# Optimization experiments

Measured on AMD Instinct MI355X. Metric: run time of the kernel, lower is better.

## Reference

```python
import jax, jax.numpy as jnp
import numpy as np

ALPHA = 0.8          # triple vs qualifier mixing weight (StarE/QUAD 'sum' strategy)
NUM_ENT = 200000
NUM_REL = 100        # base relations; with inverses rel table has 2*NUM_REL rows
E_DIR = 500000       # edges per direction; edge_index has 2*E_DIR columns
NQ_DIR = 400000      # qualifier (rel, ent, edge_id) triples per direction
D = 200              # emb_dim == gcn_dim
B = 4096             # batch of statements
QP = 6               # qualifier pairs per statement -> quals_ix is [B, 2*QP]


def setup_inputs() -> dict:
    key = jax.random.key(0)
    ks = jax.random.split(key, 24)
    f = lambda i, shape: jax.random.normal(ks[i], shape, jnp.float32) * 0.05
    inp = {
        "ent_embs": f(0, (NUM_ENT, D)),
        "rel_embs": f(1, (2 * NUM_REL, D)),
    }
    for j, n in enumerate(["w_in1", "w_out1", "w_loop1", "w_rel1", "w_q1",
                           "w_in2", "w_out2", "w_loop2", "w_rel2", "w_q2"]):
        inp[n] = f(2 + j, (D, D))
    inp["loop_rel1"] = f(12, (1, D))
    inp["loop_rel2"] = f(13, (1, D))
    inp["b1"] = jnp.zeros((D,), jnp.float32)
    inp["b2"] = jnp.zeros((D,), jnp.float32)
    src = jax.random.randint(ks[14], (E_DIR,), 0, NUM_ENT)
    dst = jax.random.randint(ks[15], (E_DIR,), 0, NUM_ENT)
    # second half are inverse edges
    inp["edge_index"] = jnp.concatenate([jnp.stack([src, dst]), jnp.stack([dst, src])], axis=1)
    et = jax.random.randint(ks[16], (E_DIR,), 0, NUM_REL)
    inp["edge_type"] = jnp.concatenate([et, et + NUM_REL])
    q_r = jax.random.randint(ks[17], (2 * NQ_DIR,), 0, 2 * NUM_REL)
    q_e = jax.random.randint(ks[18], (2 * NQ_DIR,), 0, NUM_ENT)
    q_eid = jax.random.randint(ks[19], (2 * NQ_DIR,), 0, E_DIR)
    inp["quals"] = jnp.stack([q_r, q_e, q_eid])  # [3, 2*NQ_DIR]
    inp["ent_ix"] = jax.random.randint(ks[20], (B,), 0, NUM_ENT)
    inp["rel_ix"] = jax.random.randint(ks[21], (B,), 0, 2 * NUM_REL)
    qi_r = jax.random.randint(ks[22], (B, QP), 0, 2 * NUM_REL)
    qi_e = jax.random.randint(ks[23], (B, QP), 0, NUM_ENT)
    inp["quals_ix"] = jnp.stack([qi_r, qi_e], axis=-1).reshape(B, 2 * QP)  # alternating rel, ent
    return inp


def _comp(h, r):  # CompGCN 'mult' composition
    return h * r


def _compgcn_conv(x, r, edge_index, edge_type, quals,
                  w_in, w_out, w_loop, w_rel, w_q, loop_rel, bias):
    n_ent = x.shape[0]
    E = edge_index.shape[1] // 2
    NQ = quals.shape[1] // 2
    rel_all = jnp.concatenate([r, loop_rel], axis=0)  # loop relation appended last

    def one_dir(idx, etype, q_r, q_e, q_eid, w):
        src, dst = idx[0], idx[1]
        # qualifier-aware per-edge relation embedding
        q_msg = _comp(x[q_e], rel_all[q_r])                               # [NQ, d]
        q_agg = jax.ops.segment_sum(q_msg, q_eid, num_segments=E)        # scatter-sum onto edges
        rel_e = ALPHA * rel_all[etype] + (1.0 - ALPHA) * (q_agg @ w_q)   # [E, d]
        msg = _comp(x[src], rel_e) @ w                                   # [E, d_out]
        deg = jax.ops.segment_sum(jnp.ones((E,), x.dtype), src, num_segments=n_ent)
        dinv = jnp.where(deg > 0, jax.lax.rsqrt(jnp.maximum(deg, 1.0)), 0.0)
        norm = dinv[src] * dinv[dst]                                     # sym degree norm
        return jax.ops.segment_sum(norm[:, None] * msg, dst, num_segments=n_ent)

    in_res = one_dir(edge_index[:, :E], edge_type[:E],
                     quals[0, :NQ], quals[1, :NQ], quals[2, :NQ], w_in)
    out_res = one_dir(edge_index[:, E:], edge_type[E:],
                      quals[0, NQ:], quals[1, NQ:], quals[2, NQ:], w_out)
    loop_res = _comp(x, loop_rel) @ w_loop
    out = (in_res + out_res + loop_res) / 3.0 + bias
    return jnp.tanh(out), rel_all[:-1] @ w_rel


def reference(ent_embs, rel_embs,
              w_in1, w_out1, w_loop1, w_rel1, w_q1, loop_rel1, b1,
              w_in2, w_out2, w_loop2, w_rel2, w_q2, loop_rel2, b2,
              edge_index, edge_type, quals, ent_ix, rel_ix, quals_ix):
    x, r = _compgcn_conv(ent_embs, rel_embs, edge_index, edge_type, quals,
                         w_in1, w_out1, w_loop1, w_rel1, w_q1, loop_rel1, b1)
    x, r = _compgcn_conv(x, r, edge_index, edge_type, quals,
                         w_in2, w_out2, w_loop2, w_rel2, w_q2, loop_rel2, b2)
    sub_emb = x[ent_ix]                                   # [B, d]
    rel_emb = r[rel_ix]                                   # [B, d]
    quals_ents = quals_ix[:, 1::2].reshape(-1)
    quals_rels = quals_ix[:, 0::2].reshape(-1)
    qual_obj_emb = x[quals_ents].reshape(sub_emb.shape[0], -1, sub_emb.shape[1])
    qual_rel_emb = r[quals_rels].reshape(rel_emb.shape[0], -1, rel_emb.shape[1])
    return (sub_emb, rel_emb, qual_obj_emb, qual_rel_emb, x, r)
```

## Files before the change

kernel.cpp:

```cpp
#include <hip/hip_runtime.h>
#include <cstdio>


#define ALPHA_MIX 0.8f

constexpr int N_ENT  = 200000;
constexpr int D_     = 200;
constexpr int E_DIR_ = 500000;
constexpr int NQ_    = 400000;
constexpr int B_     = 4096;

constexpr int NT_  = 13;
constexpr int LDA_ = 232;
constexpr int WLD_ = 224;

constexpr size_t OFS_SUB  = 0;
constexpr size_t OFS_REL  = 819200;
constexpr size_t OFS_QOBJ = 1638400;
constexpr size_t OFS_QREL = 6553600;
constexpr size_t OFS_X    = 11468800;
constexpr size_t OFS_R    = 51468800;

typedef __bf16 bf16x8 __attribute__((ext_vector_type(8)));
typedef float  f32x4  __attribute__((ext_vector_type(4)));

__device__ __forceinline__ unsigned int f2bf(float f) {
  unsigned int u = __float_as_uint(f);
  u += 0x7FFFu + ((u >> 16) & 1u);
  return u >> 16;
}
__device__ __forceinline__ unsigned long long pack4bf(float x, float y, float z, float w) {
  return (unsigned long long)f2bf(x) | ((unsigned long long)f2bf(y) << 16) |
         ((unsigned long long)f2bf(z) << 32) | ((unsigned long long)f2bf(w) << 48);
}
__device__ __forceinline__ float bf_lo(unsigned int u) { return __uint_as_float(u << 16); }
__device__ __forceinline__ float bf_hi(unsigned int u) { return __uint_as_float(u & 0xFFFF0000u); }
__device__ __forceinline__ unsigned int mulpk(unsigned int a, unsigned int b) {
  return f2bf(bf_lo(a) * bf_lo(b)) | (f2bf(bf_hi(a) * bf_hi(b)) << 16);
}

typedef short v2s __attribute__((ext_vector_type(2)));
__device__ __forceinline__ void atomic_pk_add_bf16(unsigned short* addr, unsigned int pk) {
#if __has_builtin(__builtin_amdgcn_global_atomic_fadd_v2bf16)
  v2s v;
  __builtin_memcpy(&v, &pk, 4);
  __builtin_amdgcn_global_atomic_fadd_v2bf16(
      (__attribute__((address_space(1))) v2s*)(unsigned long long)addr, v);
#else
  unsigned int* ap = (unsigned int*)addr;
  unsigned int old = *ap;
  while (true) {
    unsigned int nv = f2bf(bf_lo(old) + bf_lo(pk)) | (f2bf(bf_hi(old) + bf_hi(pk)) << 16);
    unsigned int prev = atomicCAS(ap, old, nv);
    if (prev == old) break;
    old = prev;
  }
#endif
}

__global__ __launch_bounds__(256)
void gemm_qual(const unsigned short* __restrict__ Xbf, const unsigned short* __restrict__ Rbf,
               const int* __restrict__ q_e, const int* __restrict__ q_r,
               const int* __restrict__ q_eid,
               const int* __restrict__ srcv, const int* __restrict__ dstv,
               const float* __restrict__ nrm,
               const unsigned short* __restrict__ Bp,
               unsigned short* __restrict__ pre, int nrows)
{
  __shared__ __align__(16) unsigned short As[64 * LDA_];
  __shared__ int s_g[64], s_r[64], s_eid[64], s_dst[64];
  __shared__ float s_nm[64];

  const int t  = threadIdx.x;
  const int r0 = blockIdx.x * 64;

  if (t < 64) {
    int cr = min(r0 + t, nrows - 1);
    s_g[t] = q_e[cr]; s_r[t] = q_r[cr]; s_eid[t] = q_eid[cr];
  }
  __syncthreads();

  for (int task = t; task < 64 * 25; task += 256) {
    int i = task / 25, c = task % 25;
    uint4 xv = ((const uint4*)(Xbf + (size_t)s_g[i] * D_))[c];
    uint4 rv = ((const uint4*)(Rbf + (size_t)s_r[i] * D_))[c];
    uint4 o;
    o.x = mulpk(xv.x, rv.x); o.y = mulpk(xv.y, rv.y);
    o.z = mulpk(xv.z, rv.z); o.w = mulpk(xv.w, rv.w);
    *(uint4*)(As + i * LDA_ + c * 8) = o;
  }
  for (int task = t; task < 64 * 3; task += 256) {
    int i = task / 3, c = task % 3;
    *(uint4*)(As + i * LDA_ + 200 + c * 8) = make_uint4(0, 0, 0, 0);
  }
  __syncthreads();

  const int wave = t >> 6, lane = t & 63;
  const int m = lane & 15, quad = lane >> 4;

  f32x4 acc[NT_];
  const f32x4 zero = {0.f, 0.f, 0.f, 0.f};
  #pragma unroll
  for (int i = 0; i < NT_; i++) acc[i] = zero;

  {
    const unsigned short* arow = As + (wave * 16 + m) * LDA_ + quad * 8;
    const unsigned short* brow = Bp + (size_t)m * WLD_ + quad * 8;
    #pragma unroll
    for (int ks = 0; ks < 7; ks++) {
      bf16x8 av = *(const bf16x8*)(arow + ks * 32);
      #pragma unroll
      for (int tt = 0; tt < NT_; tt++) {
        bf16x8 bv = *(const bf16x8*)(brow + (size_t)tt * 16 * WLD_ + ks * 32);
        acc[tt] = __builtin_amdgcn_mfma_f32_16x16x32_bf16(av, bv, acc[tt], 0, 0, 0);
      }
    }
  }

  __syncthreads();
  if (t < 64) {
    int e = s_eid[t];
    s_dst[t] = dstv[e];
    s_nm[t]  = (1.0f - ALPHA_MIX) * nrm[e];
    s_g[t]   = srcv[e];
  }
  __syncthreads();
  for (int task = t; task < 64 * 25; task += 256) {
    int i = task / 25, c = task % 25;
    *(uint4*)(As + i * LDA_ + c * 8) = ((const uint4*)(Xbf + (size_t)s_g[i] * D_))[c];
  }
  __syncthreads();

  #pragma unroll
  for (int rg = 0; rg < 4; rg++) {
    int row = r0 + wave * 16 + quad * 4 + rg;
    bool valid = row < nrows;
    int li = row - r0;
    size_t orow = (size_t)s_dst[li] * D_;
    float nm = s_nm[li];
    #pragma unroll
    for (int tt = 0; tt < NT_; tt++) {
      int col = tt * 16 + m;
      float xv = (col < D_) ? __uint_as_float(((unsigned int)As[li * LDA_ + col]) << 16) : 0.0f;
      float v  = acc[tt][rg] * nm * xv;
      float vn = __shfl_xor(v, 1);
      if (valid && !(m & 1) && col < D_) {
        unsigned int pk = f2bf(v) | (f2bf(vn) << 16);
        atomic_pk_add_bf16(pre + orow + col, pk);
      }
    }
  }
}

__global__ __launch_bounds__(256)
void node_gather(const int* __restrict__ starts, const int* __restrict__ csr,
                 const int* __restrict__ srcv, const int* __restrict__ et,
                 const float* __restrict__ nrm,
                 const unsigned short* __restrict__ xbf,
                 const unsigned short* __restrict__ rallbf,
                 unsigned short* __restrict__ pre)
{
  int node = blockIdx.x * 4 + (threadIdx.x >> 6);
  if (node >= N_ENT) return;
  int lane = threadIdx.x & 63;
  int p0 = starts[node], p1 = starts[node + 1];
  float a0 = 0.f, a1 = 0.f, a2 = 0.f, a3 = 0.f;
  for (int p = p0; p < p1; p++) {
    int e = csr[p];
    int s = srcv[e], ty = et[e];
    float nm = nrm[e];
    if (lane < 50) {
      uint2 xv = ((const uint2*)(xbf + (size_t)s * D_))[lane];
      uint2 rv = ((const uint2*)(rallbf + (size_t)ty * D_))[lane];
      a0 += nm * bf_lo(xv.x) * bf_lo(rv.x);
      a1 += nm * bf_hi(xv.x) * bf_hi(rv.x);
      a2 += nm * bf_lo(xv.y) * bf_lo(rv.y);
      a3 += nm * bf_hi(xv.y) * bf_hi(rv.y);
    }
  }
  if (lane < 50) {
    uint2 o;
    o.x = f2bf(a0 * ALPHA_MIX) | (f2bf(a1 * ALPHA_MIX) << 16);
    o.y = f2bf(a2 * ALPHA_MIX) | (f2bf(a3 * ALPHA_MIX) << 16);
    ((uint2*)(pre + (size_t)node * D_))[lane] = o;
  }
}

__global__ __launch_bounds__(256)
void gemm_node(const unsigned short* __restrict__ pre0,
               const unsigned short* __restrict__ pre1,
               const unsigned short* __restrict__ xbf,
               const unsigned short* __restrict__ lrel,
               const unsigned short* __restrict__ B0,
               const unsigned short* __restrict__ B1,
               const unsigned short* __restrict__ B2,
               const float* __restrict__ bias,
               float* __restrict__ xo, unsigned short* __restrict__ xbf_out,
               int nrows)
{
  __shared__ __align__(16) unsigned short As[64 * LDA_];
  const int t  = threadIdx.x;
  const int r0 = blockIdx.x * 64;

  for (int task = t; task < 64 * 3; task += 256) {
    int i = task / 3, c = task % 3;
    *(uint4*)(As + i * LDA_ + 200 + c * 8) = make_uint4(0, 0, 0, 0);
  }

  const int wave = t >> 6, lane = t & 63;
  const int m = lane & 15, quad = lane >> 4;

  f32x4 acc[NT_];
  const f32x4 zero = {0.f, 0.f, 0.f, 0.f};
  #pragma unroll
  for (int i = 0; i < NT_; i++) acc[i] = zero;

  const unsigned short* Asrc[3] = {pre0, pre1, xbf};
  const unsigned short* Bsel[3] = {B0, B1, B2};

  #pragma unroll
  for (int seg = 0; seg < 3; seg++) {
    __syncthreads();
    for (int task = t; task < 64 * 25; task += 256) {
      int i = task / 25, c = task % 25;
      int cr = min(r0 + i, nrows - 1);
      uint4 vv = ((const uint4*)(Asrc[seg] + (size_t)cr * D_))[c];
      if (seg == 2) {
        uint4 lv = ((const uint4*)lrel)[c];
        vv.x = mulpk(vv.x, lv.x); vv.y = mulpk(vv.y, lv.y);
        vv.z = mulpk(vv.z, lv.z); vv.w = mulpk(vv.w, lv.w);
      }
      *(uint4*)(As + i * LDA_ + c * 8) = vv;
    }
    __syncthreads();

    const unsigned short* arow = As + (wave * 16 + m) * LDA_ + quad * 8;
    const unsigned short* brow = Bsel[seg] + (size_t)m * WLD_ + quad * 8;
    #pragma unroll
    for (int ks = 0; ks < 7; ks++) {
      bf16x8 av = *(const bf16x8*)(arow + ks * 32);
      #pragma unroll
      for (int tt = 0; tt < NT_; tt++) {
        bf16x8 bv = *(const bf16x8*)(brow + (size_t)tt * 16 * WLD_ + ks * 32);
        acc[tt] = __builtin_amdgcn_mfma_f32_16x16x32_bf16(av, bv, acc[tt], 0, 0, 0);
      }
    }
  }

  #pragma unroll
  for (int rg = 0; rg < 4; rg++) {
    int row = r0 + wave * 16 + quad * 4 + rg;
    if (row < nrows) {
      #pragma unroll
      for (int tt = 0; tt < NT_; tt++) {
        int col = tt * 16 + m;
        if (col < D_) {
          float v = acc[tt][rg] * (1.0f / 3.0f) + bias[col];
          float th = tanhf(v);
          if (xo) xo[(size_t)row * D_ + col] = th;
          xbf_out[(size_t)row * D_ + col] = (unsigned short)f2bf(th);
        }
      }
    }
  }
}

__global__ __launch_bounds__(256)
void gemm_rel200(const float* __restrict__ X, const unsigned short* __restrict__ Bp,
                 float* __restrict__ Out, int nrows)
{
  __shared__ __align__(16) unsigned short As[64 * LDA_];
  const int t  = threadIdx.x;
  const int r0 = blockIdx.x * 64;

  for (int task = t; task < 64 * 50; task += 256) {
    int i = task / 50, c = task % 50;
    int cr = min(r0 + i, nrows - 1);
    float4 xv = ((const float4*)(X + (size_t)cr * D_))[c];
    *(unsigned long long*)&As[i * LDA_ + c * 4] = pack4bf(xv.x, xv.y, xv.z, xv.w);
  }
  for (int task = t; task < 64 * 6; task += 256) {
    int i = task / 6, c = task % 6;
    *(unsigned long long*)&As[i * LDA_ + 200 + c * 4] = 0ull;
  }
  __syncthreads();

  const int wave = t >> 6, lane = t & 63;
  const int m = lane & 15, quad = lane >> 4;

  f32x4 acc[NT_];
  const f32x4 zero = {0.f, 0.f, 0.f, 0.f};
  #pragma unroll
  for (int i = 0; i < NT_; i++) acc[i] = zero;

  const unsigned short* arow = As + (wave * 16 + m) * LDA_ + quad * 8;
  const unsigned short* brow = Bp + (size_t)m * WLD_ + quad * 8;
  #pragma unroll
  for (int ks = 0; ks < 7; ks++) {
    bf16x8 av = *(const bf16x8*)(arow + ks * 32);
    #pragma unroll
    for (int tt = 0; tt < NT_; tt++) {
      bf16x8 bv = *(const bf16x8*)(brow + (size_t)tt * 16 * WLD_ + ks * 32);
      acc[tt] = __builtin_amdgcn_mfma_f32_16x16x32_bf16(av, bv, acc[tt], 0, 0, 0);
    }
  }

  #pragma unroll
  for (int rg = 0; rg < 4; rg++) {
    int row = r0 + wave * 16 + quad * 4 + rg;
    if (row < nrows) {
      #pragma unroll
      for (int tt = 0; tt < NT_; tt++) {
        int col = tt * 16 + m;
        if (col < D_) Out[(size_t)row * D_ + col] = acc[tt][rg];
      }
    }
  }
}

struct WP10 { const float* p[10]; };

__global__ void convert_weights(WP10 wp, unsigned short* __restrict__ wbp) {
  int i = blockIdx.x * 256 + threadIdx.x;
  if (i < 10 * 208 * WLD_) {
    int j = i / (208 * WLD_);
    int rem = i % (208 * WLD_);
    int n = rem / WLD_, k = rem % WLD_;
    float v = (n < D_ && k < D_) ? wp.p[j][(size_t)k * D_ + n] : 0.0f;
    wbp[i] = (unsigned short)f2bf(v);
  }
}

__global__ void conv_f32_bf16_vec(const float* __restrict__ src,
                                  unsigned short* __restrict__ dst, int n4) {
  int i = blockIdx.x * 256 + threadIdx.x;
  if (i < n4) {
    float4 v = ((const float4*)src)[i];
    uint2 o;
    o.x = f2bf(v.x) | (f2bf(v.y) << 16);
    o.y = f2bf(v.z) | (f2bf(v.w) << 16);
    ((uint2*)dst)[i] = o;
  }
}

__global__ void build_rall(const float* __restrict__ rel_embs,
                           const float* __restrict__ loop_rel,
                           float* __restrict__ rall) {
  int i = blockIdx.x * 256 + threadIdx.x;
  if (i < 201 * D_) rall[i] = (i < 200 * D_) ? rel_embs[i] : loop_rel[i - 200 * D_];
}

__global__ void copy_row(const float* __restrict__ src, float* __restrict__ dst, int n) {
  int i = blockIdx.x * 256 + threadIdx.x;
  if (i < n) dst[i] = src[i];
}

__global__ void deg_count(const int* __restrict__ src, int* __restrict__ deg, int E) {
  int e = blockIdx.x * 256 + threadIdx.x;
  if (e < E) atomicAdd(&deg[src[e]], 1);
}

__global__ void norm_build(const int* __restrict__ src, const int* __restrict__ dst,
                           const int* __restrict__ deg, float* __restrict__ nrm, int E) {
  int e = blockIdx.x * 256 + threadIdx.x;
  if (e < E) {
    int a = deg[src[e]], b = deg[dst[e]];
    float fa = (a > 0) ? rsqrtf((float)a) : 0.0f;
    float fb = (b > 0) ? rsqrtf((float)b) : 0.0f;
    nrm[e] = fa * fb;
  }
}

constexpr int SCHUNK = 2048;

__global__ void scan_partial(const int* __restrict__ in, int* __restrict__ part, int n) {
  __shared__ int red[256];
  int b = blockIdx.x, t = threadIdx.x;
  int base = b * SCHUNK + t * 8;
  int s = 0;
  #pragma unroll
  for (int j = 0; j < 8; j++) { int i = base + j; if (i < n) s += in[i]; }
  red[t] = s; __syncthreads();
  for (int off = 128; off > 0; off >>= 1) {
    if (t < off) red[t] += red[t + off];
    __syncthreads();
  }
  if (t == 0) part[b] = red[0];
}

__global__ void scan_part_seq(int* part, int nb) {
  if (threadIdx.x == 0 && blockIdx.x == 0) {
    int run = 0;
    for (int i = 0; i < nb; i++) { int v = part[i]; part[i] = run; run += v; }
  }
}

__global__ void scan_final(const int* __restrict__ in, const int* __restrict__ part,
                           int* __restrict__ outs, int* __restrict__ cursor,
                           int n, int total) {
  __shared__ int buf[256];
  int b = blockIdx.x, t = threadIdx.x;
  int base = b * SCHUNK + t * 8;
  int v[8]; int s = 0;
  #pragma unroll
  for (int j = 0; j < 8; j++) { int i = base + j; v[j] = (i < n) ? in[i] : 0; s += v[j]; }
  buf[t] = s; __syncthreads();
  for (int off = 1; off < 256; off <<= 1) {
    int add = (t >= off) ? buf[t - off] : 0;
    __syncthreads();
    buf[t] += add;
    __syncthreads();
  }
  int excl = buf[t] - s + part[b];
  #pragma unroll
  for (int j = 0; j < 8; j++) {
    int i = base + j;
    if (i < n) { outs[i] = excl; cursor[i] = excl; }
    excl += v[j];
  }
  if (b == 0 && t == 0) outs[n] = total;
}

__global__ void fill_csr(const int* __restrict__ dstv, int* __restrict__ cursor,
                         int* __restrict__ csr, int E) {
  int e = blockIdx.x * 256 + threadIdx.x;
  if (e < E) {
    int pos = atomicAdd(&cursor[dstv[e]], 1);
    csr[pos] = e;
  }
}

__global__ void gather_out(const float* __restrict__ x2, const float* __restrict__ r2,
                           const int* __restrict__ ent_ix, const int* __restrict__ rel_ix,
                           const int* __restrict__ quals_ix, float* __restrict__ out) {
  int i = blockIdx.x * 256 + threadIdx.x;
  if (i >= B_ * 14 * 50) return;
  int b = i / 700, rem = i % 700, slot = rem / 50, c = rem % 50;
  const float* srcrow; float* dstrow;
  if (slot == 0)      { srcrow = x2 + (size_t)ent_ix[b] * D_;  dstrow = out + OFS_SUB + (size_t)b * D_; }
  else if (slot == 1) { srcrow = r2 + (size_t)rel_ix[b] * D_;  dstrow = out + OFS_REL + (size_t)b * D_; }
  else if (slot < 8)  { int j = slot - 2;
                        srcrow = x2 + (size_t)quals_ix[b * 12 + 2 * j + 1] * D_;
                        dstrow = out + OFS_QOBJ + ((size_t)b * 6 + j) * D_; }
  else                { int j = slot - 8;
                        srcrow = r2 + (size_t)quals_ix[b * 12 + 2 * j] * D_;
                        dstrow = out + OFS_QREL + ((size_t)b * 6 + j) * D_; }
  ((float4*)dstrow)[c] = ((const float4*)srcrow)[c];
}

extern "C" void kernel_launch(void* const* d_in, const int* in_sizes, int n_in,
                              void* d_out, int out_size, void* d_ws, size_t ws_size,
                              hipStream_t stream)
{
  const float* ent       = (const float*)d_in[0];
  const float* rel_embs  = (const float*)d_in[1];
  const float* loop_rel1 = (const float*)d_in[12];
  const float* loop_rel2 = (const float*)d_in[13];
  const float* b1        = (const float*)d_in[14];
  const float* b2        = (const float*)d_in[15];
  const int*   ei        = (const int*)d_in[16];
  const int*   etype     = (const int*)d_in[17];
  const int*   quals     = (const int*)d_in[18];
  const int*   ent_ix    = (const int*)d_in[19];
  const int*   rel_ix    = (const int*)d_in[20];
  const int*   quals_ix  = (const int*)d_in[21];

  char* wsb = (char*)d_ws;
  size_t off = 0;
  auto walloc = [&](size_t bytes) -> char* {
    char* p = wsb + off; off += (bytes + 511) & ~(size_t)511; return p;
  };
  unsigned short* pre0  = (unsigned short*)walloc((size_t)N_ENT * D_ * 2);
  unsigned short* pre1  = (unsigned short*)walloc((size_t)N_ENT * D_ * 2);
  unsigned short* x_bf  = (unsigned short*)walloc((size_t)N_ENT * D_ * 2);
  float* norm1 = (float*)walloc((size_t)E_DIR_ * 4);
  float* norm2 = (float*)walloc((size_t)E_DIR_ * 4);
  int*   degA  = (int*)walloc((size_t)N_ENT * 4);
  int*   degB  = (int*)walloc((size_t)N_ENT * 4);
  int*   starts0 = (int*)walloc((size_t)(N_ENT + 1) * 4);
  int*   starts1 = (int*)walloc((size_t)(N_ENT + 1) * 4);
  int*   cursor0 = (int*)walloc((size_t)N_ENT * 4);
  int*   cursor1 = (int*)walloc((size_t)N_ENT * 4);
  int*   csr0    = (int*)walloc((size_t)E_DIR_ * 4);
  int*   csr1    = (int*)walloc((size_t)E_DIR_ * 4);
  int*   part    = (int*)walloc((size_t)256 * 4);
  float* rall1 = (float*)walloc((size_t)201 * D_ * 4);
  float* rall2 = (float*)walloc((size_t)201 * D_ * 4);
  unsigned short* rall1_bf = (unsigned short*)walloc((size_t)201 * D_ * 2);
  unsigned short* rall2_bf = (unsigned short*)walloc((size_t)201 * D_ * 2);
  unsigned short* lrel1_bf = (unsigned short*)walloc((size_t)D_ * 2);
  unsigned short* lrel2_bf = (unsigned short*)walloc((size_t)D_ * 2);
  unsigned short* wbp = (unsigned short*)walloc((size_t)10 * 208 * WLD_ * 2);
  if (off > ws_size) fprintf(stderr, "ws overflow: need %zu have %zu\n", off, ws_size);

  float* out   = (float*)d_out;
  float* x_out = out + OFS_X;
  float* r_out = out + OFS_R;

  auto WB = [&](int j) { return wbp + (size_t)j * 208 * WLD_; };

  WP10 wp; for (int j = 0; j < 10; j++) wp.p[j] = (const float*)d_in[2 + j];
  convert_weights<<<(10 * 208 * WLD_ + 255) / 256, 256, 0, stream>>>(wp, wbp);
  build_rall<<<(201 * D_ + 255) / 256, 256, 0, stream>>>(rel_embs, loop_rel1, rall1);
  conv_f32_bf16_vec<<<(201 * 50 + 255) / 256, 256, 0, stream>>>(rall1, rall1_bf, 201 * 50);
  conv_f32_bf16_vec<<<(N_ENT * 50 + 255) / 256, 256, 0, stream>>>(ent, x_bf, N_ENT * 50);
  conv_f32_bf16_vec<<<1, 256, 0, stream>>>(loop_rel1, lrel1_bf, 50);
  conv_f32_bf16_vec<<<1, 256, 0, stream>>>(loop_rel2, lrel2_bf, 50);

  const int* src1 = ei;
  const int* dst1 = ei + 2 * E_DIR_;
  const int* src2 = ei + E_DIR_;
  const int* dst2 = ei + 3 * E_DIR_;

  int gE = (E_DIR_ + 255) / 256;
  hipMemsetAsync(degA, 0, (size_t)N_ENT * 4, stream);
  hipMemsetAsync(degB, 0, (size_t)N_ENT * 4, stream);
  deg_count<<<gE, 256, 0, stream>>>(src1, degA, E_DIR_);
  deg_count<<<gE, 256, 0, stream>>>(src2, degB, E_DIR_);
  norm_build<<<gE, 256, 0, stream>>>(src1, dst1, degA, norm1, E_DIR_);
  norm_build<<<gE, 256, 0, stream>>>(src2, dst2, degB, norm2, E_DIR_);

  int nbScan = (N_ENT + SCHUNK - 1) / SCHUNK;
  scan_partial<<<nbScan, 256, 0, stream>>>(degB, part, N_ENT);
  scan_part_seq<<<1, 64, 0, stream>>>(part, nbScan);
  scan_final<<<nbScan, 256, 0, stream>>>(degB, part, starts0, cursor0, N_ENT, E_DIR_);
  fill_csr<<<gE, 256, 0, stream>>>(dst1, cursor0, csr0, E_DIR_);

  scan_partial<<<nbScan, 256, 0, stream>>>(degA, part, N_ENT);
  scan_part_seq<<<1, 64, 0, stream>>>(part, nbScan);
  scan_final<<<nbScan, 256, 0, stream>>>(degA, part, starts1, cursor1, N_ENT, E_DIR_);
  fill_csr<<<gE, 256, 0, stream>>>(dst2, cursor1, csr1, E_DIR_);

  const int* q_r   = quals;
  const int* q_e   = quals + 2 * NQ_;
  const int* q_eid = quals + 4 * NQ_;

  for (int layer = 0; layer < 2; layer++) {
    const float* rallf = layer ? rall2 : rall1;
    const unsigned short* rallbf = layer ? rall2_bf : rall1_bf;
    const unsigned short* lrelbf = layer ? lrel2_bf : lrel1_bf;
    const float* bias = layer ? b2 : b1;
    const unsigned short* w_q    = WB(layer ? 9 : 4);
    const unsigned short* w_loop = WB(layer ? 7 : 2);
    const unsigned short* w_rel  = WB(layer ? 8 : 3);
    const unsigned short* w_in   = WB(layer ? 5 : 0);
    const unsigned short* w_out  = WB(layer ? 6 : 1);

    float* r_dst = layer ? r_out : rall2;
    gemm_rel200<<<4, 256, 0, stream>>>(rallf, w_rel, r_dst, 200);
    if (layer == 0) {
      copy_row<<<1, 256, 0, stream>>>(loop_rel2, rall2 + (size_t)200 * D_, D_);
      conv_f32_bf16_vec<<<(201 * 50 + 255) / 256, 256, 0, stream>>>(rall2, rall2_bf, 201 * 50);
    }

    for (int dir = 0; dir < 2; dir++) {
      const int* et  = etype + dir * E_DIR_;
      const int* qr  = q_r + dir * NQ_;
      const int* qe  = q_e + dir * NQ_;
      const int* qid = q_eid + dir * NQ_;
      const int* s   = dir ? src2 : src1;
      const int* dd  = dir ? dst2 : dst1;
      const float* nm = dir ? norm2 : norm1;
      const int* sts = dir ? starts1 : starts0;
      const int* csr = dir ? csr1 : csr0;
      unsigned short* pre = dir ? pre1 : pre0;

      node_gather<<<(N_ENT + 3) / 4, 256, 0, stream>>>(sts, csr, s, et, nm, x_bf, rallbf, pre);
      gemm_qual<<<(NQ_ + 63) / 64, 256, 0, stream>>>(x_bf, rallbf, qe, qr, qid,
                                                     s, dd, nm, w_q, pre, NQ_);
    }

    gemm_node<<<(N_ENT + 63) / 64, 256, 0, stream>>>(
        pre0, pre1, x_bf, lrelbf, w_in, w_out, w_loop, bias,
        layer ? x_out : (float*)nullptr, x_bf, N_ENT);
  }

  gather_out<<<(B_ * 14 * 50 + 255) / 256, 256, 0, stream>>>(
      x_out, r_out, ent_ix, rel_ix, quals_ix, out);
}
```

Before: 3.388 ms.

## Prefetch gather rows into registers to overlap global loads with MFMA

In gemm_qual, the edge metadata (dst, src, norm) is now loaded up front, and the source-row gather for the epilogue is issued into registers before the first GEMM, so it is no longer a serialized phase after the GEMM. In gemm_node, the next segment's A tile (pre1, then xbf) is prefetched into registers while MFMAs on the current segment run, with a sched_barrier to keep the loads ahead of the compute. This hides global-load latency but raises register pressure (7 uint4 per thread plus 52 accumulators), which could lower occupancy or cause spills.

```diff
diff --git a/kernel.cpp b/kernel.cpp
--- a/kernel.cpp
+++ b/kernel.cpp
@@ -68,7 +68,7 @@
                unsigned short* __restrict__ pre, int nrows)
 {
   __shared__ __align__(16) unsigned short As[64 * LDA_];
-  __shared__ int s_g[64], s_r[64], s_eid[64], s_dst[64];
+  __shared__ int s_g[64], s_r[64], s_src[64], s_dst[64];
   __shared__ float s_nm[64];
 
   const int t  = threadIdx.x;
@@ -76,18 +76,40 @@
 
   if (t < 64) {
     int cr = min(r0 + t, nrows - 1);
-    s_g[t] = q_e[cr]; s_r[t] = q_r[cr]; s_eid[t] = q_eid[cr];
-  }
+    s_g[t] = q_e[cr]; s_r[t] = q_r[cr];
+    int e = q_eid[cr];
+    s_dst[t] = dstv[e];
+    s_src[t] = srcv[e];
+    s_nm[t]  = (1.0f - ALPHA_MIX) * nrm[e];
+  }
+
+  int ti[7], tc[7];
+  #pragma unroll
+  for (int j = 0; j < 7; j++) {
+    if (j < 6 || t < 64) {
+      int task = t + j * 256;
+      ti[j] = task / 25; tc[j] = task % 25;
+    }
+  }
+
   __syncthreads();
 
-  for (int task = t; task < 64 * 25; task += 256) {
-    int i = task / 25, c = task % 25;
-    uint4 xv = ((const uint4*)(Xbf + (size_t)s_g[i] * D_))[c];
-    uint4 rv = ((const uint4*)(Rbf + (size_t)s_r[i] * D_))[c];
-    uint4 o;
-    o.x = mulpk(xv.x, rv.x); o.y = mulpk(xv.y, rv.y);
-    o.z = mulpk(xv.z, rv.z); o.w = mulpk(xv.w, rv.w);
-    *(uint4*)(As + i * LDA_ + c * 8) = o;
+  uint4 rx[7];
+  #pragma unroll
+  for (int j = 0; j < 7; j++)
+    if (j < 6 || t < 64)
+      rx[j] = ((const uint4*)(Xbf + (size_t)s_src[ti[j]] * D_))[tc[j]];
+
+  #pragma unroll
+  for (int j = 0; j < 7; j++) {
+    if (j < 6 || t < 64) {
+      uint4 xv = ((const uint4*)(Xbf + (size_t)s_g[ti[j]] * D_))[tc[j]];
+      uint4 rv = ((const uint4*)(Rbf + (size_t)s_r[ti[j]] * D_))[tc[j]];
+      uint4 o;
+      o.x = mulpk(xv.x, rv.x); o.y = mulpk(xv.y, rv.y);
+      o.z = mulpk(xv.z, rv.z); o.w = mulpk(xv.w, rv.w);
+      *(uint4*)(As + ti[j] * LDA_ + tc[j] * 8) = o;
+    }
   }
   for (int task = t; task < 64 * 3; task += 256) {
     int i = task / 3, c = task % 3;
@@ -118,17 +140,10 @@
   }
 
   __syncthreads();
-  if (t < 64) {
-    int e = s_eid[t];
-    s_dst[t] = dstv[e];
-    s_nm[t]  = (1.0f - ALPHA_MIX) * nrm[e];
-    s_g[t]   = srcv[e];
-  }
-  __syncthreads();
-  for (int task = t; task < 64 * 25; task += 256) {
-    int i = task / 25, c = task % 25;
-    *(uint4*)(As + i * LDA_ + c * 8) = ((const uint4*)(Xbf + (size_t)s_g[i] * D_))[c];
-  }
+  #pragma unroll
+  for (int j = 0; j < 7; j++)
+    if (j < 6 || t < 64)
+      *(uint4*)(As + ti[j] * LDA_ + tc[j] * 8) = rx[j];
   __syncthreads();
 
   #pragma unroll
@@ -202,6 +217,22 @@
   const int t  = threadIdx.x;
   const int r0 = blockIdx.x * 64;
 
+  int ti[7], tc[7];
+  size_t trow[7];
+  #pragma unroll
+  for (int j = 0; j < 7; j++) {
+    if (j < 6 || t < 64) {
+      int task = t + j * 256;
+      ti[j] = task / 25; tc[j] = task % 25;
+      trow[j] = (size_t)min(r0 + ti[j], nrows - 1) * D_;
+    }
+  }
+
+  uint4 rv[7];
+  #pragma unroll
+  for (int j = 0; j < 7; j++)
+    if (j < 6 || t < 64) rv[j] = ((const uint4*)(pre0 + trow[j]))[tc[j]];
+
   for (int task = t; task < 64 * 3; task += 256) {
     int i = task / 3, c = task % 3;
     *(uint4*)(As + i * LDA_ + 200 + c * 8) = make_uint4(0, 0, 0, 0);
@@ -215,24 +246,34 @@
   #pragma unroll
   for (int i = 0; i < NT_; i++) acc[i] = zero;
 
-  const unsigned short* Asrc[3] = {pre0, pre1, xbf};
   const unsigned short* Bsel[3] = {B0, B1, B2};
 
   #pragma unroll
   for (int seg = 0; seg < 3; seg++) {
+    #pragma unroll
+    for (int j = 0; j < 7; j++) {
+      if (j < 6 || t < 64) {
+        uint4 vv = rv[j];
+        if (seg == 2) {
+          uint4 lv = ((const uint4*)lrel)[tc[j]];
+          vv.x = mulpk(vv.x, lv.x); vv.y = mulpk(vv.y, lv.y);
+          vv.z = mulpk(vv.z, lv.z); vv.w = mulpk(vv.w, lv.w);
+        }
+        *(uint4*)(As + ti[j] * LDA_ + tc[j] * 8) = vv;
+      }
+    }
     __syncthreads();
-    for (int task = t; task < 64 * 25; task += 256) {
-      int i = task / 25, c = task % 25;
-      int cr = min(r0 + i, nrows - 1);
-      uint4 vv = ((const uint4*)(Asrc[seg] + (size_t)cr * D_))[c];
-      if (seg == 2) {
-        uint4 lv = ((const uint4*)lrel)[c];
-        vv.x = mulpk(vv.x, lv.x); vv.y = mulpk(vv.y, lv.y);
-        vv.z = mulpk(vv.z, lv.z); vv.w = mulpk(vv.w, lv.w);
-      }
-      *(uint4*)(As + i * LDA_ + c * 8) = vv;
-    }
-    __syncthreads();
+
+    if (seg == 0) {
+      #pragma unroll
+      for (int j = 0; j < 7; j++)
+        if (j < 6 || t < 64) rv[j] = ((const uint4*)(pre1 + trow[j]))[tc[j]];
+    } else if (seg == 1) {
+      #pragma unroll
+      for (int j = 0; j < 7; j++)
+        if (j < 6 || t < 64) rv[j] = ((const uint4*)(xbf + trow[j]))[tc[j]];
+    }
+    __builtin_amdgcn_sched_barrier(0);
 
     const unsigned short* arow = As + (wave * 16 + m) * LDA_ + quad * 8;
     const unsigned short* brow = Bsel[seg] + (size_t)m * WLD_ + quad * 8;
@@ -245,6 +286,7 @@
         acc[tt] = __builtin_amdgcn_mfma_f32_16x16x32_bf16(av, bv, acc[tt], 0, 0, 0);
       }
     }
+    __syncthreads();
   }
 
   #pragma unroll
```

After: 3.982 ms. +17.5%, slower.

## Restructure node GEMM: stage weight column slice in LDS, A fragments in registers

Applied to the files above, without the earlier changes.

The node GEMM now splits output columns into three parts, and each 512-thread block stages its column slice of all three weight matrices in shared memory. A operands are loaded straight from global memory into registers instead of through shared memory. Each block then loops over a group of 16-row tiles, so B reuse is high and the per-segment syncs go away. It also swaps tanhf for an exp2/rcp approximation, and it double-buffers the bf16 x so the layer-0 output no longer overwrites its own input. The trade-off is that A rows are read three times, once per column part.

```diff
diff --git a/kernel.cpp b/kernel.cpp
--- a/kernel.cpp
+++ b/kernel.cpp
@@ -13,6 +13,9 @@
 constexpr int NT_  = 13;
 constexpr int LDA_ = 232;
 constexpr int WLD_ = 224;
+constexpr int SB_  = 232;
+constexpr int PB_  = 80;
+constexpr int NTILES_ = (N_ENT + 15) / 16;
 
 constexpr size_t OFS_SUB  = 0;
 constexpr size_t OFS_REL  = 819200;
@@ -37,6 +40,11 @@
 __device__ __forceinline__ float bf_hi(unsigned int u) { return __uint_as_float(u & 0xFFFF0000u); }
 __device__ __forceinline__ unsigned int mulpk(unsigned int a, unsigned int b) {
   return f2bf(bf_lo(a) * bf_lo(b)) | (f2bf(bf_hi(a) * bf_hi(b)) << 16);
+}
+__device__ __forceinline__ float fast_tanh(float x) {
+  float xx = fminf(fmaxf(x, -9.0f), 9.0f);
+  float e = __builtin_amdgcn_exp2f(xx * 2.8853900817779268f);
+  return (e - 1.0f) * __builtin_amdgcn_rcpf(e + 1.0f);
 }
 
 typedef short v2s __attribute__((ext_vector_type(2)));
@@ -186,83 +194,120 @@
   }
 }
 
-__global__ __launch_bounds__(256)
+template<int NTH>
+__device__ __forceinline__ void node_core(
+    const unsigned short* Bl,
+    const unsigned short* __restrict__ pre0,
+    const unsigned short* __restrict__ pre1,
+    const unsigned short* __restrict__ xsrc,
+    const uint4* lv,
+    const float* __restrict__ bias,
+    float* __restrict__ xo, unsigned short* __restrict__ xbo,
+    int rowblk, int wave, int m, int quad, int ncol0, int nrows)
+{
+  for (int i = wave; i < 49; i += 8) {
+    int T = rowblk * 49 + i;
+    if (T >= NTILES_) break;
+    int rowi = min(T * 16 + m, nrows - 1);
+    const unsigned short* a0 = pre0 + (size_t)rowi * D_ + quad * 8;
+    const unsigned short* a1 = pre1 + (size_t)rowi * D_ + quad * 8;
+    const unsigned short* a2 = xsrc + (size_t)rowi * D_ + quad * 8;
+
+    uint4 af[3][7];
+    #pragma unroll
+    for (int ks = 0; ks < 7; ks++) af[0][ks] = *(const uint4*)(a0 + ks * 32);
+    #pragma unroll
+    for (int ks = 0; ks < 7; ks++) af[1][ks] = *(const uint4*)(a1 + ks * 32);
+    #pragma unroll
+    for (int ks = 0; ks < 7; ks++) af[2][ks] = *(const uint4*)(a2 + ks * 32);
+
+    f32x4 acc[NTH];
+    const f32x4 zero = {0.f, 0.f, 0.f, 0.f};
+    #pragma unroll
+    for (int tt = 0; tt < NTH; tt++) acc[tt] = zero;
+
+    #pragma unroll
+    for (int seg = 0; seg < 3; seg++) {
+      #pragma unroll
+      for (int ks = 0; ks < 7; ks++) {
+        uint4 a = af[seg][ks];
+        if (seg == 2) {
+          a.x = mulpk(a.x, lv[ks].x); a.y = mulpk(a.y, lv[ks].y);
+          a.z = mulpk(a.z, lv[ks].z); a.w = mulpk(a.w, lv[ks].w);
+        }
+        bf16x8 av; __builtin_memcpy(&av, &a, 16);
+        #pragma unroll
+        for (int tt = 0; tt < NTH; tt++) {
+          const unsigned short* bp = Bl + (size_t)(seg * PB_ + tt * 16 + m) * SB_ + quad * 8 + ks * 32;
+          bf16x8 bv = *(const bf16x8*)bp;
+          acc[tt] = __builtin_amdgcn_mfma_f32_16x16x32_bf16(av, bv, acc[tt], 0, 0, 0);
+        }
+      }
+    }
+
+    #pragma unroll
+    for (int rg = 0; rg < 4; rg++) {
+      int row = T * 16 + quad * 4 + rg;
+      if (row < nrows) {
+        #pragma unroll
+        for (int tt = 0; tt < NTH; tt++) {
+          int col = ncol0 + tt * 16 + m;
+          if (col < D_) {
+            float v = acc[tt][rg] * (1.0f / 3.0f) + bias[col];
+            float th = fast_tanh(v);
+            if (xo)  xo[(size_t)row * D_ + col] = th;
+            if (xbo) xbo[(size_t)row * D_ + col] = (unsigned short)f2bf(th);
+          }
+        }
+      }
+    }
+  }
+}
+
+__global__ __launch_bounds__(512)
 void gemm_node(const unsigned short* __restrict__ pre0,
                const unsigned short* __restrict__ pre1,
-               const unsigned short* __restrict__ xbf,
+               const unsigned short* __restrict__ xsrc,
                const unsigned short* __restrict__ lrel,
                const unsigned short* __restrict__ B0,
                const unsigned short* __restrict__ B1,
                const unsigned short* __restrict__ B2,
                const float* __restrict__ bias,
-               float* __restrict__ xo, unsigned short* __restrict__ xbf_out,
+               float* __restrict__ xo, unsigned short* __restrict__ xbo,
                int nrows)
 {
-  __shared__ __align__(16) unsigned short As[64 * LDA_];
-  const int t  = threadIdx.x;
-  const int r0 = blockIdx.x * 64;
-
-  for (int task = t; task < 64 * 3; task += 256) {
-    int i = task / 3, c = task % 3;
-    *(uint4*)(As + i * LDA_ + 200 + c * 8) = make_uint4(0, 0, 0, 0);
-  }
+  __shared__ __align__(16) unsigned short Bl[3 * PB_ * SB_];
+  const int t   = threadIdx.x;
+  const int bid = blockIdx.x;
+  const int x8 = bid & 7, q = bid >> 3;
+  const int part   = q % 3;
+  const int rowblk = (q / 3) * 8 + x8;
+  const int nth    = (part == 2) ? 3 : 5;
+  const int ncol0  = part * PB_;
+  const int nrB    = nth * 16;
+
+  const unsigned short* Bs[3] = {B0, B1, B2};
+  for (int task = t; task < 3 * nrB * 28; task += 512) {
+    int seg = task / (nrB * 28);
+    int rem = task % (nrB * 28);
+    int n = rem / 28, c = rem % 28;
+    uint4 v = *(const uint4*)(Bs[seg] + (size_t)(ncol0 + n) * WLD_ + c * 8);
+    *(uint4*)(Bl + (size_t)(seg * PB_ + n) * SB_ + c * 8) = v;
+  }
+  __syncthreads();
 
   const int wave = t >> 6, lane = t & 63;
   const int m = lane & 15, quad = lane >> 4;
 
-  f32x4 acc[NT_];
-  const f32x4 zero = {0.f, 0.f, 0.f, 0.f};
-  #pragma unroll
-  for (int i = 0; i < NT_; i++) acc[i] = zero;
-
-  const unsigned short* Asrc[3] = {pre0, pre1, xbf};
-  const unsigned short* Bsel[3] = {B0, B1, B2};
-
-  #pragma unroll
-  for (int seg = 0; seg < 3; seg++) {
-    __syncthreads();
-    for (int task = t; task < 64 * 25; task += 256) {
-      int i = task / 25, c = task % 25;
-      int cr = min(r0 + i, nrows - 1);
-      uint4 vv = ((const uint4*)(Asrc[seg] + (size_t)cr * D_))[c];
-      if (seg == 2) {
-        uint4 lv = ((const uint4*)lrel)[c];
-        vv.x = mulpk(vv.x, lv.x); vv.y = mulpk(vv.y, lv.y);
-        vv.z = mulpk(vv.z, lv.z); vv.w = mulpk(vv.w, lv.w);
-      }
-      *(uint4*)(As + i * LDA_ + c * 8) = vv;
-    }
-    __syncthreads();
-
-    const unsigned short* arow = As + (wave * 16 + m) * LDA_ + quad * 8;
-    const unsigned short* brow = Bsel[seg] + (size_t)m * WLD_ + quad * 8;
-    #pragma unroll
-    for (int ks = 0; ks < 7; ks++) {
-      bf16x8 av = *(const bf16x8*)(arow + ks * 32);
-      #pragma unroll
-      for (int tt = 0; tt < NT_; tt++) {
-        bf16x8 bv = *(const bf16x8*)(brow + (size_t)tt * 16 * WLD_ + ks * 32);
-        acc[tt] = __builtin_amdgcn_mfma_f32_16x16x32_bf16(av, bv, acc[tt], 0, 0, 0);
-      }
-    }
-  }
-
-  #pragma unroll
-  for (int rg = 0; rg < 4; rg++) {
-    int row = r0 + wave * 16 + quad * 4 + rg;
-    if (row < nrows) {
-      #pragma unroll
-      for (int tt = 0; tt < NT_; tt++) {
-        int col = tt * 16 + m;
-        if (col < D_) {
-          float v = acc[tt][rg] * (1.0f / 3.0f) + bias[col];
-          float th = tanhf(v);
-          if (xo) xo[(size_t)row * D_ + col] = th;
-          xbf_out[(size_t)row * D_ + col] = (unsigned short)f2bf(th);
-        }
-      }
-    }
-  }
+  uint4 lv[7];
+  #pragma unroll
+  for (int ks = 0; ks < 7; ks++)
+    lv[ks] = *(const uint4*)(lrel + quad * 8 + ks * 32);
+
+  if (part == 2)
+    node_core<3>(Bl, pre0, pre1, xsrc, lv, bias, xo, xbo, rowblk, wave, m, quad, ncol0, nrows);
+  else
+    node_core<5>(Bl, pre0, pre1, xsrc, lv, bias, xo, xbo, rowblk, wave, m, quad, ncol0, nrows);
 }
 
 __global__ __launch_bounds__(256)
@@ -473,6 +518,7 @@
   unsigned short* pre0  = (unsigned short*)walloc((size_t)N_ENT * D_ * 2);
   unsigned short* pre1  = (unsigned short*)walloc((size_t)N_ENT * D_ * 2);
   unsigned short* x_bf  = (unsigned short*)walloc((size_t)N_ENT * D_ * 2);
+  unsigned short* xb2   = (unsigned short*)walloc((size_t)N_ENT * D_ * 2);
   float* norm1 = (float*)walloc((size_t)E_DIR_ * 4);
   float* norm2 = (float*)walloc((size_t)E_DIR_ * 4);
   int*   degA  = (int*)walloc((size_t)N_ENT * 4);
@@ -545,6 +591,7 @@
     const unsigned short* w_rel  = WB(layer ? 8 : 3);
     const unsigned short* w_in   = WB(layer ? 5 : 0);
     const unsigned short* w_out  = WB(layer ? 6 : 1);
+    const unsigned short* xin    = layer ? xb2 : x_bf;
 
     float* r_dst = layer ? r_out : rall2;
     gemm_rel200<<<4, 256, 0, stream>>>(rallf, w_rel, r_dst, 200);
@@ -565,14 +612,19 @@
       const int* csr = dir ? csr1 : csr0;
       unsigned short* pre = dir ? pre1 : pre0;
 
-      node_gather<<<(N_ENT + 3) / 4, 256, 0, stream>>>(sts, csr, s, et, nm, x_bf, rallbf, pre);
-      gemm_qual<<<(NQ_ + 63) / 64, 256, 0, stream>>>(x_bf, rallbf, qe, qr, qid,
+      node_gather<<<(N_ENT + 3) / 4, 256, 0, stream>>>(sts, csr, s, et, nm, xin, rallbf, pre);
+      gemm_qual<<<(NQ_ + 63) / 64, 256, 0, stream>>>(xin, rallbf, qe, qr, qid,
                                                      s, dd, nm, w_q, pre, NQ_);
     }
 
-    gemm_node<<<(N_ENT + 63) / 64, 256, 0, stream>>>(
-        pre0, pre1, x_bf, lrelbf, w_in, w_out, w_loop, bias,
-        layer ? x_out : (float*)nullptr, x_bf, N_ENT);
+    if (layer == 0)
+      gemm_node<<<768, 512, 0, stream>>>(pre0, pre1, xin, lrelbf,
+                                         w_in, w_out, w_loop, bias,
+                                         (float*)nullptr, xb2, N_ENT);
+    else
+      gemm_node<<<768, 512, 0, stream>>>(pre0, pre1, xin, lrelbf,
+                                         w_in, w_out, w_loop, bias,
+                                         x_out, (unsigned short*)nullptr, N_ENT);
   }
 
   gather_out<<<(B_ * 14 * 50 + 255) / 256, 256, 0, stream>>>(
```

After: 2.962 ms. -12.6%, faster.
